# Performance work log

Measured on AMD Instinct MI355X. Metric: run time of the kernel, lower is better.

Reference implementation:

```python
import jax, jax.numpy as jnp
import numpy as np

N_NODES = 100000
N_EDGES = 1600000
N_GRAPHS = 64
IN_DIM, HID, OUT_DIM = 64, 128, 32


def _glorot(key, shape):
    lim = float(np.sqrt(6.0 / (shape[0] + shape[1])))
    return jax.random.uniform(key, shape, jnp.float32, -lim, lim)


def setup_inputs() -> dict:
    key = jax.random.key(0)
    ks = jax.random.split(key, 20)
    x = jax.random.normal(ks[0], (N_NODES, IN_DIM), jnp.float32)
    edge_index = jax.random.randint(ks[1], (2, N_EDGES), 0, N_NODES, jnp.int64)
    batch = jnp.sort(jax.random.randint(ks[2], (N_NODES,), 0, N_GRAPHS, jnp.int64))
    d = {"x": x, "edge_index": edge_index, "batch": batch}
    dims = [(IN_DIM, HID), (HID, HID), (HID, HID), (HID, HID), (HID, OUT_DIM)]
    names = ["W1", "W2", "W3", "W4", "Wo"]
    bnames = ["b1", "b2", "b3", "b4", "bo"]
    for i, ((di, do), wn, bn) in enumerate(zip(dims, names, bnames)):
        d[wn] = _glorot(ks[3 + i], (di, do))
        d[bn] = jnp.zeros((do,), jnp.float32)
    # MLP: 32 -> 64 -> 8 -> 8  (hidden_dim//2, output_dim//2, output_dim//4)
    mdims = [(OUT_DIM, HID // 2), (HID // 2, OUT_DIM // 2), (OUT_DIM // 2, OUT_DIM // 4)]
    for i, (di, do) in enumerate(mdims):
        d[f"M{i+1}w"] = _glorot(ks[10 + i], (di, do))
        d[f"M{i+1}b"] = jnp.zeros((do,), jnp.float32)
    return d


def _gcn(x, src, dst, norm, W, b, n):
    h = x @ W                                    # [N, d_out] dense GEMM
    msg = h[src] * norm[:, None]                 # gather + normalize
    agg = jax.ops.segment_sum(msg, dst, num_segments=n)  # scatter-add
    return agg + b


def reference(x, edge_index, batch, W1, b1, W2, b2, W3, b3, W4, b4, Wo, bo,
              M1w, M1b, M2w, M2b, M3w, M3b):
    n = x.shape[0]
    # add self loops (PyG GCNConv default)
    loops = jnp.arange(n, dtype=edge_index.dtype)
    src = jnp.concatenate([edge_index[0], loops])
    dst = jnp.concatenate([edge_index[1], loops])
    # symmetric degree normalization: D^{-1/2} (A+I) D^{-1/2}
    deg = jax.ops.segment_sum(jnp.ones_like(src, dtype=x.dtype), dst, num_segments=n)
    dinv = jnp.where(deg > 0, jax.lax.rsqrt(deg), 0.0)
    norm = dinv[src] * dinv[dst]                 # [E+N]

    h = jax.nn.relu(_gcn(x, src, dst, norm, W1, b1, n))
    for W, b in ((W2, b2), (W3, b3), (W4, b4)):
        h = jax.nn.relu(_gcn(h, src, dst, norm, W, b, n))
    h = _gcn(h, src, dst, norm, Wo, bo, n)       # [N, 32]

    # global mean pool over graphs
    sums = jax.ops.segment_sum(h, batch, num_segments=N_GRAPHS)
    cnts = jax.ops.segment_sum(jnp.ones((n,), h.dtype), batch, num_segments=N_GRAPHS)
    g = sums / jnp.maximum(cnts, 1.0)[:, None]   # [G, 32]

    g = jax.nn.relu(g @ M1w + M1b)
    g = jax.nn.relu(g @ M2w + M2b)
    return g @ M3w + M3b                          # [G, 8]
```

## Files before the change

kernel.cpp:

```cpp
#include <hip/hip_runtime.h>


static constexpr int TPB = 256;
static constexpr int NBKT = 128;
static constexpr int NCHK = 256;
static constexpr int TILE = 2048;

using f32x4  = __attribute__((ext_vector_type(4))) float;
using bf16x8 = __attribute__((ext_vector_type(8))) short;

__device__ __forceinline__ float u2f(unsigned u) { return __uint_as_float(u); }

__device__ __forceinline__ unsigned short bf1(float a) {
    unsigned u = __float_as_uint(a);
    u += 0x7FFFu + ((u >> 16) & 1u);
    return (unsigned short)(u >> 16);
}

__device__ __forceinline__ unsigned bf2(float a, float b) {
    unsigned ua = __float_as_uint(a);
    unsigned ub = __float_as_uint(b);
    ua += 0x7FFFu + ((ua >> 16) & 1u);
    ub += 0x7FFFu + ((ub >> 16) & 1u);
    return (ua >> 16) | (ub & 0xFFFF0000u);
}

__global__ __launch_bounds__(256) void k_hist(const int* __restrict__ dst,
                                              int* __restrict__ histT, int E, int CS) {
    __shared__ int h[NBKT];
    int c = blockIdx.x, t = threadIdx.x;
    if (t < NBKT) h[t] = 0;
    __syncthreads();
    int e0 = c * CS, e1 = min(e0 + CS, E);
    for (int e = e0 + t; e < e1; e += 256)
        atomicAdd(&h[dst[e] >> 10], 1);
    __syncthreads();
    if (t < NBKT) histT[t * NCHK + c] = h[t];
}

__global__ __launch_bounds__(256) void k_scanS(const int* __restrict__ histT,
                                               int* __restrict__ stg) {
    constexpr int TOT = NBKT * NCHK;
    constexpr int PER = TOT / 256;
    __shared__ int s[256];
    int t = threadIdx.x;
    int base = t * PER;
    int sum = 0;
    for (int i = 0; i < PER; ++i) sum += histT[base + i];
    s[t] = sum;
    __syncthreads();
    for (int off = 1; off < 256; off <<= 1) {
        int add = (t >= off) ? s[t - off] : 0;
        __syncthreads();
        s[t] += add;
        __syncthreads();
    }
    int run = (t > 0) ? s[t - 1] : 0;
    for (int i = 0; i < PER; ++i) {
        stg[base + i] = run;
        run += histT[base + i];
    }
}

__global__ __launch_bounds__(256) void k_bucket(const int* __restrict__ src,
                                                const int* __restrict__ dst,
                                                const int* __restrict__ stg,
                                                unsigned* __restrict__ staging,
                                                int E, int CS) {
    __shared__ int gcur[NBKT];
    __shared__ int cnt_[NBKT];
    __shared__ int base[NBKT];
    __shared__ unsigned sval[TILE];
    __shared__ unsigned char sbkt[TILE];
    int c = blockIdx.x, t = threadIdx.x;
    if (t < NBKT) gcur[t] = stg[t * NCHK + c];
    int e0 = c * CS, e1 = min(e0 + CS, E);

    for (int tb = e0; tb < e1; tb += TILE) {
        int m = min(TILE, e1 - tb);
        __syncthreads();
        if (t < NBKT) cnt_[t] = 0;
        __syncthreads();
        int  b_[8]; unsigned v_[8]; int o_[8]; bool ok_[8];
#pragma unroll
        for (int k = 0; k < 8; ++k) {
            int e = tb + t + k * 256;
            ok_[k] = (e < tb + m);
            b_[k] = 0; v_[k] = 0; o_[k] = 0;
            if (ok_[k]) {
                int d = dst[e];
                b_[k] = d >> 10;
                v_[k] = ((unsigned)src[e] << 10) | (unsigned)(d & 1023);
                o_[k] = atomicAdd(&cnt_[b_[k]], 1);
            }
        }
        __syncthreads();
        if (t < NBKT) base[t] = cnt_[t];
        __syncthreads();
        for (int off = 1; off < NBKT; off <<= 1) {
            int v = (t < NBKT && t >= off) ? base[t - off] : 0;
            __syncthreads();
            if (t < NBKT) base[t] += v;
            __syncthreads();
        }
        if (t < NBKT) base[t] -= cnt_[t];
        __syncthreads();
#pragma unroll
        for (int k = 0; k < 8; ++k) {
            if (ok_[k]) {
                int p = base[b_[k]] + o_[k];
                sval[p] = v_[k];
                sbkt[p] = (unsigned char)b_[k];
            }
        }
        __syncthreads();
        for (int i = t; i < m; i += 256) {
            int b = sbkt[i];
            staging[gcur[b] + (i - base[b])] = sval[i];
        }
        __syncthreads();
        if (t < NBKT) gcur[t] += cnt_[t];
    }
}

__global__ __launch_bounds__(256) void k_deg(const unsigned* __restrict__ staging,
                                             const int* __restrict__ stg,
                                             int* __restrict__ cnt, int E, int n) {
    __shared__ int deg[1024];
    int r = blockIdx.x, t = threadIdx.x;
    for (int i = t; i < 1024; i += 256) deg[i] = 0;
    __syncthreads();
    int s0 = stg[r * NCHK];
    int s1 = (r == NBKT - 1) ? E : stg[(r + 1) * NCHK];
    for (int e = s0 + t; e < s1; e += 256)
        atomicAdd(&deg[staging[e] & 1023u], 1);
    __syncthreads();
    int b = r << 10;
    for (int i = t; i < 1024; i += 256)
        if (b + i < n) cnt[b + i] = deg[i];
}

__global__ void k_scanA(const int* __restrict__ cnt, int* __restrict__ rowptr,
                        int* __restrict__ bsum, int n) {
    __shared__ int s[TPB];
    int t = threadIdx.x;
    int i = blockIdx.x * TPB + t;
    s[t] = (i < n) ? cnt[i] : 0;
    __syncthreads();
    for (int off = 1; off < TPB; off <<= 1) {
        int add = (t >= off) ? s[t - off] : 0;
        __syncthreads();
        s[t] += add;
        __syncthreads();
    }
    if (i < n) rowptr[i + 1] = s[t];
    if (t == TPB - 1) bsum[blockIdx.x] = s[t];
}

__global__ void k_scanB(const int* __restrict__ bsum, int* __restrict__ bscan, int nb) {
    __shared__ int s[512];
    int t = threadIdx.x;
    s[t] = (t < nb) ? bsum[t] : 0;
    __syncthreads();
    for (int off = 1; off < 512; off <<= 1) {
        int add = (t >= off) ? s[t - off] : 0;
        __syncthreads();
        s[t] += add;
        __syncthreads();
    }
    if (t < nb) bscan[t] = (t > 0) ? s[t - 1] : 0;
}

__global__ void k_scanC(int* __restrict__ rowptr, const int* __restrict__ bscan,
                        const int* __restrict__ cnt, float* __restrict__ dinv, int n) {
    int i = blockIdx.x * blockDim.x + threadIdx.x;
    if (i >= n) return;
    rowptr[i + 1] += bscan[i >> 8];
    dinv[i] = rsqrtf((float)cnt[i] + 1.0f);
    if (i == 0) rowptr[0] = 0;
}

__global__ __launch_bounds__(256) void k_fill2(const unsigned* __restrict__ staging,
                                               const int* __restrict__ stg,
                                               const int* __restrict__ rowptr,
                                               int* __restrict__ csr, int E, int n) {
    __shared__ int cur[1024];
    int r = blockIdx.x, t = threadIdx.x;
    int b = r << 10;
    for (int i = t; i < 1024; i += 256)
        cur[i] = (b + i < n) ? rowptr[b + i] : 0;
    __syncthreads();
    int s0 = stg[r * NCHK];
    int s1 = (r == NBKT - 1) ? E : stg[(r + 1) * NCHK];
    for (int e = s0 + t; e < s1; e += 256) {
        unsigned sd = staging[e];
        int p = atomicAdd(&cur[sd & 1023u], 1);
        csr[p] = (int)(sd >> 10);
    }
}

__global__ void k_castx(const float* __restrict__ x, const float* __restrict__ dinv,
                        unsigned short* __restrict__ xs, int n) {
    int gid = blockIdx.x * blockDim.x + threadIdx.x;
    if (gid >= n * 8) return;
    int row = gid >> 3;
    float d = dinv[row];
    const float4* xp = (const float4*)x + (size_t)gid * 2;
    float4 a = xp[0], b = xp[1];
    uint4 o;
    o.x = bf2(a.x * d, a.y * d);
    o.y = bf2(a.z * d, a.w * d);
    o.z = bf2(b.x * d, b.y * d);
    o.w = bf2(b.z * d, b.w * d);
    ((uint4*)xs)[gid] = o;
}

__global__ void k_prepw(const float* __restrict__ W1, const float* __restrict__ W2,
                        const float* __restrict__ W3, const float* __restrict__ W4,
                        const float* __restrict__ Wo,
                        unsigned short* __restrict__ wt1, unsigned short* __restrict__ wt2,
                        unsigned short* __restrict__ wt3, unsigned short* __restrict__ wt4,
                        unsigned short* __restrict__ wto) {
    int b = blockIdx.x, k = threadIdx.x;
    const float* W; unsigned short* wt; int K, OUT, nn;
    if (b < 128)      { W = W1; wt = wt1; K = 64;  OUT = 128; nn = b; }
    else if (b < 256) { W = W2; wt = wt2; K = 128; OUT = 128; nn = b - 128; }
    else if (b < 384) { W = W3; wt = wt3; K = 128; OUT = 128; nn = b - 256; }
    else if (b < 512) { W = W4; wt = wt4; K = 128; OUT = 128; nn = b - 384; }
    else              { W = Wo; wt = wto; K = 128; OUT = 32;  nn = b - 512; }
    if (nn >= OUT || k >= K) return;
    float v = W[(size_t)k * OUT + nn];
    unsigned short hi = bf1(v);
    float fhi = u2f((unsigned)hi << 16);
    unsigned short lo = bf1(v - fhi);
    wt[nn * K + k] = hi;
    wt[OUT * K + nn * K + k] = lo;
}

template <int K, int OUT, int EPI>
__global__ __launch_bounds__(256) void k_gemm_mfma(
    const unsigned short* __restrict__ Ain,
    const unsigned short* __restrict__ WT,
    const float* __restrict__ dinv,
    const float* __restrict__ bias,
    unsigned short* __restrict__ out, int n) {
    constexpr int NT = OUT / 16;
    constexpr int KT = K / 32;
    constexpr int CH = K / 8;
    __shared__ __align__(16) unsigned short Wl[2 * OUT * K];

    int t = threadIdx.x;
    {
        const uint4* wg = (const uint4*)WT;
        uint4* wl = (uint4*)Wl;
        for (int i = t; i < 2 * OUT * CH; i += 256) {
            int m = i / (OUT * CH);
            int r = i - m * (OUT * CH);
            int nn = r / CH, g = r - nn * CH;
            wl[m * OUT * CH + nn * CH + (g ^ (nn & 7))] = wg[i];
        }
    }

    int wid = t >> 6, lane = t & 63;
    int lr = lane & 15, lg = lane >> 4;
    int mbase = blockIdx.x * 128 + wid * 32;

    bf16x8 a[2][KT];
#pragma unroll
    for (int mt = 0; mt < 2; ++mt) {
        int row = mbase + mt * 16 + lr;
        row = row < n ? row : n - 1;
        const bf16x8* ap = (const bf16x8*)(Ain + (size_t)row * K);
#pragma unroll
        for (int kt = 0; kt < KT; ++kt)
            a[mt][kt] = ap[kt * 4 + lg];
    }

    __syncthreads();

    f32x4 acc[2][NT] = {};
#pragma unroll
    for (int nt = 0; nt < NT; ++nt) {
        int nn = nt * 16 + lr;
        int swz = nn & 7;
        int rowoff = nn * K;
#pragma unroll
        for (int kt = 0; kt < KT; ++kt) {
            int g = kt * 4 + lg;
            int off = rowoff + ((g ^ swz) * 8);
            bf16x8 bhi = *(const bf16x8*)&Wl[off];
            bf16x8 blo = *(const bf16x8*)&Wl[OUT * K + off];
#pragma unroll
            for (int mt = 0; mt < 2; ++mt) {
                acc[mt][nt] = __builtin_amdgcn_mfma_f32_16x16x32_bf16(
                    a[mt][kt], bhi, acc[mt][nt], 0, 0, 0);
                acc[mt][nt] = __builtin_amdgcn_mfma_f32_16x16x32_bf16(
                    a[mt][kt], blo, acc[mt][nt], 0, 0, 0);
            }
        }
    }

#pragma unroll
    for (int mt = 0; mt < 2; ++mt) {
        int rbase = mbase + mt * 16 + lg * 4;
        float dv[4];
        if (EPI == 0) {
#pragma unroll
            for (int r = 0; r < 4; ++r)
                dv[r] = (rbase + r < n) ? dinv[rbase + r] : 0.f;
        }
#pragma unroll
        for (int nt = 0; nt < NT; ++nt) {
            int col = nt * 16 + lr;
            float bb = (EPI == 1) ? bias[col] : 0.f;
#pragma unroll
            for (int r = 0; r < 4; ++r) {
                int row = rbase + r;
                if (row < n) {
                    float v = acc[mt][nt][r];
                    if (EPI == 0) v *= dv[r];
                    else v = fmaxf(v + bb, 0.f);
                    out[(size_t)row * OUT + col] = bf1(v);
                }
            }
        }
    }
}

__device__ __forceinline__ void addbf(float* acc, uint4 w) {
    acc[0] += u2f(w.x << 16); acc[1] += u2f(w.x & 0xFFFF0000u);
    acc[2] += u2f(w.y << 16); acc[3] += u2f(w.y & 0xFFFF0000u);
    acc[4] += u2f(w.z << 16); acc[5] += u2f(w.z & 0xFFFF0000u);
    acc[6] += u2f(w.w << 16); acc[7] += u2f(w.w & 0xFFFF0000u);
}

template <int D, bool RELU, bool HASBIAS, bool OUTBF>
__global__ __launch_bounds__(256) void k_gather_bf(const unsigned short* __restrict__ hsb,
                                                   const int* __restrict__ rowptr,
                                                   const int* __restrict__ csr,
                                                   const float* __restrict__ dinv,
                                                   const float* __restrict__ bias,
                                                   void* __restrict__ outp, int n) {
    constexpr int TPN = D / 8;
    int gid = blockIdx.x * blockDim.x + threadIdx.x;
    int node = gid / TPN;
    if (node >= n) return;
    int c = gid % TPN;
    const uint4* hb = (const uint4*)hsb;

    float acc[8];
    {
        uint4 v = hb[(size_t)node * TPN + c];
        acc[0] = u2f(v.x << 16); acc[1] = u2f(v.x & 0xFFFF0000u);
        acc[2] = u2f(v.y << 16); acc[3] = u2f(v.y & 0xFFFF0000u);
        acc[4] = u2f(v.z << 16); acc[5] = u2f(v.z & 0xFFFF0000u);
        acc[6] = u2f(v.w << 16); acc[7] = u2f(v.w & 0xFFFF0000u);
    }
    int j0 = rowptr[node], j1 = rowptr[node + 1];
    int j = j0;
    for (; j + 3 < j1; j += 4) {
        int s0 = csr[j], s1 = csr[j + 1], s2 = csr[j + 2], s3 = csr[j + 3];
        uint4 w0 = hb[(size_t)s0 * TPN + c];
        uint4 w1 = hb[(size_t)s1 * TPN + c];
        uint4 w2 = hb[(size_t)s2 * TPN + c];
        uint4 w3 = hb[(size_t)s3 * TPN + c];
        addbf(acc, w0); addbf(acc, w1); addbf(acc, w2); addbf(acc, w3);
    }
    for (; j < j1; ++j) {
        uint4 w0 = hb[(size_t)csr[j] * TPN + c];
        addbf(acc, w0);
    }

    float di = dinv[node];
    float r[8];
    if (HASBIAS) {
        float4 b0 = *(const float4*)&bias[c * 8];
        float4 b1 = *(const float4*)&bias[c * 8 + 4];
        r[0] = di * acc[0] + b0.x; r[1] = di * acc[1] + b0.y;
        r[2] = di * acc[2] + b0.z; r[3] = di * acc[3] + b0.w;
        r[4] = di * acc[4] + b1.x; r[5] = di * acc[5] + b1.y;
        r[6] = di * acc[6] + b1.z; r[7] = di * acc[7] + b1.w;
    } else {
#pragma unroll
        for (int i = 0; i < 8; ++i) r[i] = di * acc[i];
    }
    if (RELU) {
#pragma unroll
        for (int i = 0; i < 8; ++i) r[i] = fmaxf(r[i], 0.f);
    }
    if (OUTBF) {
        uint4 o;
        o.x = bf2(r[0], r[1]); o.y = bf2(r[2], r[3]);
        o.z = bf2(r[4], r[5]); o.w = bf2(r[6], r[7]);
        ((uint4*)outp)[(size_t)node * TPN + c] = o;
    } else {
        float4 o0 = {r[0], r[1], r[2], r[3]};
        float4 o1 = {r[4], r[5], r[6], r[7]};
        float4* op = (float4*)outp + (size_t)node * TPN * 2 + c * 2;
        op[0] = o0;
        op[1] = o1;
    }
}

__global__ __launch_bounds__(256) void k_pool(const float* __restrict__ h,
                                              const int* __restrict__ batch,
                                              float* __restrict__ g, int n) {
    __shared__ int se[2];
    __shared__ float red[8][32];
    int gi = blockIdx.x;
    int t = threadIdx.x;
    if (t == 0) {
        int lo = 0, hi = n;
        while (lo < hi) { int m = (lo + hi) >> 1; if (batch[m] < gi) lo = m + 1; else hi = m; }
        se[0] = lo;
        lo = 0; hi = n;
        while (lo < hi) { int m = (lo + hi) >> 1; if (batch[m] < gi + 1) lo = m + 1; else hi = m; }
        se[1] = lo;
    }
    __syncthreads();
    int start = se[0], end = se[1];
    int col = t & 31, sub = t >> 5;
    float acc = 0.f;
    for (int i = start + sub; i < end; i += 8)
        acc += h[(size_t)i * 32 + col];
    red[sub][col] = acc;
    __syncthreads();
    if (t < 32) {
        float s = 0.f;
#pragma unroll
        for (int q = 0; q < 8; ++q) s += red[q][t];
        float c = (float)(end - start);
        g[gi * 32 + t] = s / fmaxf(c, 1.0f);
    }
}

template <int K, int O, bool RELU>
__global__ void k_mlp(const float* __restrict__ in, const float* __restrict__ W,
                      const float* __restrict__ b, float* __restrict__ out, int G) {
    int gid = blockIdx.x * blockDim.x + threadIdx.x;
    if (gid >= G * O) return;
    int g = gid / O, j = gid % O;
    float s = b[j];
    for (int k = 0; k < K; ++k) s += in[g * K + k] * W[k * O + j];
    if (RELU) s = fmaxf(s, 0.f);
    out[gid] = s;
}

extern "C" void kernel_launch(void* const* d_in, const int* in_sizes, int n_in,
                              void* d_out, int out_size, void* d_ws, size_t ws_size,
                              hipStream_t stream) {
    const float* x    = (const float*)d_in[0];
    const int*   ei   = (const int*)d_in[1];
    const int*   batch= (const int*)d_in[2];
    const float* W1 = (const float*)d_in[3];  const float* b1 = (const float*)d_in[4];
    const float* W2 = (const float*)d_in[5];  const float* b2 = (const float*)d_in[6];
    const float* W3 = (const float*)d_in[7];  const float* b3 = (const float*)d_in[8];
    const float* W4 = (const float*)d_in[9];  const float* b4 = (const float*)d_in[10];
    const float* Wo = (const float*)d_in[11]; const float* bo = (const float*)d_in[12];
    const float* M1w = (const float*)d_in[13]; const float* M1b = (const float*)d_in[14];
    const float* M2w = (const float*)d_in[15]; const float* M2b = (const float*)d_in[16];
    const float* M3w = (const float*)d_in[17]; const float* M3b = (const float*)d_in[18];

    const int N = in_sizes[0] / 64;
    const int E = in_sizes[1] / 2;
    const int G = out_size / 8;
    const int* src  = ei;
    const int* dstp = ei + E;

    char* w = (char*)d_ws;
    unsigned short* buf1 = (unsigned short*)w; w += (size_t)N * 128 * 2;
    unsigned short* buf2 = (unsigned short*)w; w += (size_t)N * 128 * 4;
    unsigned short* hsb  = (unsigned short*)w; w += (size_t)N * 128 * 2;
    int*      csr     = (int*)w;      w += (size_t)E * 4;
    unsigned* staging = (unsigned*)w; w += (size_t)E * 4;
    int*      histT   = (int*)w;      w += NBKT * NCHK * 4;
    int*      stg     = (int*)w;      w += NBKT * NCHK * 4;
    int*      cnt     = (int*)w;      w += (size_t)N * 4;
    int*      rowptr  = (int*)w;      w += (size_t)(N + 4) * 4;
    int*      bsum    = (int*)w;      w += 4096;
    int*      bscan   = (int*)w;      w += 4096;
    float*    dinv    = (float*)w;    w += (size_t)N * 4;
    unsigned short* wt1 = (unsigned short*)w; w += 2 * 128 * 64 * 2;
    unsigned short* wt2 = (unsigned short*)w; w += 2 * 128 * 128 * 2;
    unsigned short* wt3 = (unsigned short*)w; w += 2 * 128 * 128 * 2;
    unsigned short* wt4 = (unsigned short*)w; w += 2 * 128 * 128 * 2;
    unsigned short* wto = (unsigned short*)w; w += 2 * 32 * 128 * 2;
    float*    gp      = (float*)w;    w += 64 * 32 * 4;
    float*    m1      = (float*)w;    w += 64 * 64 * 4;
    float*    m2      = (float*)w;    w += 64 * 16 * 4;

    const int NB = (N + TPB - 1) / TPB;
    const int CS = (E + NCHK - 1) / NCHK;
    const int GB = (N + 127) / 128;

    k_hist<<<NCHK, 256, 0, stream>>>(dstp, histT, E, CS);
    k_prepw<<<544, 128, 0, stream>>>(W1, W2, W3, W4, Wo, wt1, wt2, wt3, wt4, wto);
    k_scanS<<<1, 256, 0, stream>>>(histT, stg);
    k_bucket<<<NCHK, 256, 0, stream>>>(src, dstp, stg, staging, E, CS);
    k_deg<<<NBKT, 256, 0, stream>>>(staging, stg, cnt, E, N);
    k_scanA<<<NB, TPB, 0, stream>>>(cnt, rowptr, bsum, N);
    k_scanB<<<1, 512, 0, stream>>>(bsum, bscan, NB);
    k_scanC<<<NB, TPB, 0, stream>>>(rowptr, bscan, cnt, dinv, N);
    k_fill2<<<NBKT, 256, 0, stream>>>(staging, stg, rowptr, csr, E, N);

    unsigned short* agg = buf1;
    unsigned short* xs  = buf2;

    k_castx<<<(N * 8 + 255) / 256, 256, 0, stream>>>(x, dinv, xs, N);
    k_gather_bf<64, false, false, true><<<(N * 8 + 255) / 256, 256, 0, stream>>>(
        xs, rowptr, csr, dinv, nullptr, agg, N);
    k_gemm_mfma<64, 128, 1><<<GB, 256, 0, stream>>>(agg, wt1, nullptr, b1, buf2, N);

    k_gemm_mfma<128, 128, 0><<<GB, 256, 0, stream>>>(buf2, wt2, dinv, nullptr, hsb, N);
    k_gather_bf<128, true, true, true><<<(N * 16 + 255) / 256, 256, 0, stream>>>(
        hsb, rowptr, csr, dinv, b2, buf1, N);
    k_gemm_mfma<128, 128, 0><<<GB, 256, 0, stream>>>(buf1, wt3, dinv, nullptr, hsb, N);
    k_gather_bf<128, true, true, true><<<(N * 16 + 255) / 256, 256, 0, stream>>>(
        hsb, rowptr, csr, dinv, b3, buf2, N);
    k_gemm_mfma<128, 128, 0><<<GB, 256, 0, stream>>>(buf2, wt4, dinv, nullptr, hsb, N);
    k_gather_bf<128, true, true, true><<<(N * 16 + 255) / 256, 256, 0, stream>>>(
        hsb, rowptr, csr, dinv, b4, buf1, N);

    k_gemm_mfma<128, 32, 0><<<GB, 256, 0, stream>>>(buf1, wto, dinv, nullptr, hsb, N);
    float* hout = (float*)buf2;
    k_gather_bf<32, false, true, false><<<(N * 4 + 255) / 256, 256, 0, stream>>>(
        hsb, rowptr, csr, dinv, bo, hout, N);

    k_pool<<<G, 256, 0, stream>>>(hout, batch, gp, N);
    k_mlp<32, 64, true><<<(G * 64 + 255) / 256, 256, 0, stream>>>(gp, M1w, M1b, m1, G);
    k_mlp<64, 16, true><<<(G * 16 + 255) / 256, 256, 0, stream>>>(m1, M2w, M2b, m2, G);
    k_mlp<16, 8, false><<<(G * 8 + 255) / 256, 256, 0, stream>>>(m2, M3w, M3b, (float*)d_out, G);
}
```

Measured before the change: 628.8 us.

## Fuse CSR build into one kernel and use XCD-restricted persistent gather queue

Merges degree counting, the three-pass prefix scan and CSR fill into a single k_build kernel. This works because each bucket's node range is contiguous and its edge offset is already known from stg, so the scan can be done locally per block. It also replaces the one-thread-per-feature-chunk gather kernels with a persistent atomic work-queue kernel. Most blocks running on XCDs with ID 4 or higher exit immediately, so the gathers are intended to run on half the XCDs, which should improve L2 locality of the gathered feature rows. The risks are fewer compute units doing gather work, contention on the queue atomic, and reliance on the XCC_ID hardware register.

```diff
diff --git a/kernel.cpp b/kernel.cpp
--- a/kernel.cpp
+++ b/kernel.cpp
@@ -5,6 +5,8 @@
 static constexpr int NBKT = 128;
 static constexpr int NCHK = 256;
 static constexpr int TILE = 2048;
+static constexpr int GQ_GRID = 2048;
+static constexpr int GQ_FS   = GQ_GRID - 256;
 
 using f32x4  = __attribute__((ext_vector_type(4))) float;
 using bf16x8 = __attribute__((ext_vector_type(8))) short;
@@ -123,10 +125,13 @@
     }
 }
 
-__global__ __launch_bounds__(256) void k_deg(const unsigned* __restrict__ staging,
-                                             const int* __restrict__ stg,
-                                             int* __restrict__ cnt, int E, int n) {
+__global__ __launch_bounds__(256) void k_build(const unsigned* __restrict__ staging,
+                                               const int* __restrict__ stg,
+                                               int* __restrict__ rowptr,
+                                               float* __restrict__ dinv,
+                                               int* __restrict__ csr, int E, int n) {
     __shared__ int deg[1024];
+    __shared__ int tsum[256];
     int r = blockIdx.x, t = threadIdx.x;
     for (int i = t; i < 1024; i += 256) deg[i] = 0;
     __syncthreads();
@@ -135,66 +140,30 @@
     for (int e = s0 + t; e < s1; e += 256)
         atomicAdd(&deg[staging[e] & 1023u], 1);
     __syncthreads();
+    int d0 = deg[t * 4], d1 = deg[t * 4 + 1], d2 = deg[t * 4 + 2], d3 = deg[t * 4 + 3];
+    tsum[t] = d0 + d1 + d2 + d3;
+    __syncthreads();
+    for (int off = 1; off < 256; off <<= 1) {
+        int v = (t >= off) ? tsum[t - off] : 0;
+        __syncthreads();
+        tsum[t] += v;
+        __syncthreads();
+    }
+    int o0 = s0 + ((t > 0) ? tsum[t - 1] : 0);
+    int o1 = o0 + d0, o2 = o1 + d1, o3 = o2 + d2;
     int b = r << 10;
-    for (int i = t; i < 1024; i += 256)
-        if (b + i < n) cnt[b + i] = deg[i];
-}
-
-__global__ void k_scanA(const int* __restrict__ cnt, int* __restrict__ rowptr,
-                        int* __restrict__ bsum, int n) {
-    __shared__ int s[TPB];
-    int t = threadIdx.x;
-    int i = blockIdx.x * TPB + t;
-    s[t] = (i < n) ? cnt[i] : 0;
-    __syncthreads();
-    for (int off = 1; off < TPB; off <<= 1) {
-        int add = (t >= off) ? s[t - off] : 0;
-        __syncthreads();
-        s[t] += add;
-        __syncthreads();
-    }
-    if (i < n) rowptr[i + 1] = s[t];
-    if (t == TPB - 1) bsum[blockIdx.x] = s[t];
-}
-
-__global__ void k_scanB(const int* __restrict__ bsum, int* __restrict__ bscan, int nb) {
-    __shared__ int s[512];
-    int t = threadIdx.x;
-    s[t] = (t < nb) ? bsum[t] : 0;
-    __syncthreads();
-    for (int off = 1; off < 512; off <<= 1) {
-        int add = (t >= off) ? s[t - off] : 0;
-        __syncthreads();
-        s[t] += add;
-        __syncthreads();
-    }
-    if (t < nb) bscan[t] = (t > 0) ? s[t - 1] : 0;
-}
-
-__global__ void k_scanC(int* __restrict__ rowptr, const int* __restrict__ bscan,
-                        const int* __restrict__ cnt, float* __restrict__ dinv, int n) {
-    int i = blockIdx.x * blockDim.x + threadIdx.x;
-    if (i >= n) return;
-    rowptr[i + 1] += bscan[i >> 8];
-    dinv[i] = rsqrtf((float)cnt[i] + 1.0f);
-    if (i == 0) rowptr[0] = 0;
-}
-
-__global__ __launch_bounds__(256) void k_fill2(const unsigned* __restrict__ staging,
-                                               const int* __restrict__ stg,
-                                               const int* __restrict__ rowptr,
-                                               int* __restrict__ csr, int E, int n) {
-    __shared__ int cur[1024];
-    int r = blockIdx.x, t = threadIdx.x;
-    int b = r << 10;
-    for (int i = t; i < 1024; i += 256)
-        cur[i] = (b + i < n) ? rowptr[b + i] : 0;
-    __syncthreads();
-    int s0 = stg[r * NCHK];
-    int s1 = (r == NBKT - 1) ? E : stg[(r + 1) * NCHK];
+    int nd = b + t * 4;
+    if (nd + 0 < n) { rowptr[nd + 0] = o0; dinv[nd + 0] = rsqrtf((float)d0 + 1.f); }
+    if (nd + 1 < n) { rowptr[nd + 1] = o1; dinv[nd + 1] = rsqrtf((float)d1 + 1.f); }
+    if (nd + 2 < n) { rowptr[nd + 2] = o2; dinv[nd + 2] = rsqrtf((float)d2 + 1.f); }
+    if (nd + 3 < n) { rowptr[nd + 3] = o3; dinv[nd + 3] = rsqrtf((float)d3 + 1.f); }
+    if (r == 0 && t == 0) rowptr[n] = E;
+    __syncthreads();
+    deg[t * 4] = o0; deg[t * 4 + 1] = o1; deg[t * 4 + 2] = o2; deg[t * 4 + 3] = o3;
+    __syncthreads();
     for (int e = s0 + t; e < s1; e += 256) {
         unsigned sd = staging[e];
-        int p = atomicAdd(&cur[sd & 1023u], 1);
+        int p = atomicAdd(&deg[sd & 1023u], 1);
         csr[p] = (int)(sd >> 10);
     }
 }
@@ -334,71 +303,88 @@
     acc[6] += u2f(w.w << 16); acc[7] += u2f(w.w & 0xFFFF0000u);
 }
 
-template <int D, bool RELU, bool HASBIAS, bool OUTBF>
-__global__ __launch_bounds__(256) void k_gather_bf(const unsigned short* __restrict__ hsb,
-                                                   const int* __restrict__ rowptr,
-                                                   const int* __restrict__ csr,
-                                                   const float* __restrict__ dinv,
-                                                   const float* __restrict__ bias,
-                                                   void* __restrict__ outp, int n) {
+template <int D, bool RELU, bool HASBIAS, bool OUTBF, int NXCD>
+__global__ __launch_bounds__(256) void k_gather_q(
+    const unsigned short* __restrict__ hsb,
+    const int* __restrict__ rowptr, const int* __restrict__ csr,
+    const float* __restrict__ dinv, const float* __restrict__ bias,
+    void* __restrict__ outp, int* __restrict__ qctr, int n, int nitems) {
     constexpr int TPN = D / 8;
-    int gid = blockIdx.x * blockDim.x + threadIdx.x;
-    int node = gid / TPN;
-    if (node >= n) return;
-    int c = gid % TPN;
+    constexpr int NPB = 256 / TPN;
+    constexpr int NSTR = 2;
+    constexpr int ITEM = NPB * NSTR;
+    __shared__ int sitem;
+    unsigned xcc;
+    asm volatile("s_getreg_b32 %0, hwreg(HW_REG_XCC_ID)" : "=s"(xcc));
+    if ((int)(xcc & 7) >= NXCD && blockIdx.x < GQ_FS) return;
+    int t = threadIdx.x;
+    int c = t % TPN;
+    int nl = t / TPN;
     const uint4* hb = (const uint4*)hsb;
 
-    float acc[8];
-    {
-        uint4 v = hb[(size_t)node * TPN + c];
-        acc[0] = u2f(v.x << 16); acc[1] = u2f(v.x & 0xFFFF0000u);
-        acc[2] = u2f(v.y << 16); acc[3] = u2f(v.y & 0xFFFF0000u);
-        acc[4] = u2f(v.z << 16); acc[5] = u2f(v.z & 0xFFFF0000u);
-        acc[6] = u2f(v.w << 16); acc[7] = u2f(v.w & 0xFFFF0000u);
-    }
-    int j0 = rowptr[node], j1 = rowptr[node + 1];
-    int j = j0;
-    for (; j + 3 < j1; j += 4) {
-        int s0 = csr[j], s1 = csr[j + 1], s2 = csr[j + 2], s3 = csr[j + 3];
-        uint4 w0 = hb[(size_t)s0 * TPN + c];
-        uint4 w1 = hb[(size_t)s1 * TPN + c];
-        uint4 w2 = hb[(size_t)s2 * TPN + c];
-        uint4 w3 = hb[(size_t)s3 * TPN + c];
-        addbf(acc, w0); addbf(acc, w1); addbf(acc, w2); addbf(acc, w3);
-    }
-    for (; j < j1; ++j) {
-        uint4 w0 = hb[(size_t)csr[j] * TPN + c];
-        addbf(acc, w0);
-    }
-
-    float di = dinv[node];
-    float r[8];
-    if (HASBIAS) {
-        float4 b0 = *(const float4*)&bias[c * 8];
-        float4 b1 = *(const float4*)&bias[c * 8 + 4];
-        r[0] = di * acc[0] + b0.x; r[1] = di * acc[1] + b0.y;
-        r[2] = di * acc[2] + b0.z; r[3] = di * acc[3] + b0.w;
-        r[4] = di * acc[4] + b1.x; r[5] = di * acc[5] + b1.y;
-        r[6] = di * acc[6] + b1.z; r[7] = di * acc[7] + b1.w;
-    } else {
-#pragma unroll
-        for (int i = 0; i < 8; ++i) r[i] = di * acc[i];
-    }
-    if (RELU) {
-#pragma unroll
-        for (int i = 0; i < 8; ++i) r[i] = fmaxf(r[i], 0.f);
-    }
-    if (OUTBF) {
-        uint4 o;
-        o.x = bf2(r[0], r[1]); o.y = bf2(r[2], r[3]);
-        o.z = bf2(r[4], r[5]); o.w = bf2(r[6], r[7]);
-        ((uint4*)outp)[(size_t)node * TPN + c] = o;
-    } else {
-        float4 o0 = {r[0], r[1], r[2], r[3]};
-        float4 o1 = {r[4], r[5], r[6], r[7]};
-        float4* op = (float4*)outp + (size_t)node * TPN * 2 + c * 2;
-        op[0] = o0;
-        op[1] = o1;
+    for (;;) {
+        if (t == 0) sitem = atomicAdd(qctr, 1);
+        __syncthreads();
+        int item = sitem;
+        __syncthreads();
+        if (item >= nitems) return;
+#pragma unroll
+        for (int s = 0; s < NSTR; ++s) {
+            int node = item * ITEM + s * NPB + nl;
+            if (node >= n) continue;
+            float acc[8];
+            {
+                uint4 v = hb[(size_t)node * TPN + c];
+                acc[0] = u2f(v.x << 16); acc[1] = u2f(v.x & 0xFFFF0000u);
+                acc[2] = u2f(v.y << 16); acc[3] = u2f(v.y & 0xFFFF0000u);
+                acc[4] = u2f(v.z << 16); acc[5] = u2f(v.z & 0xFFFF0000u);
+                acc[6] = u2f(v.w << 16); acc[7] = u2f(v.w & 0xFFFF0000u);
+            }
+            int j0 = rowptr[node], j1 = rowptr[node + 1];
+            int j = j0;
+            for (; j + 3 < j1; j += 4) {
+                int s0 = csr[j], s1 = csr[j + 1], s2 = csr[j + 2], s3 = csr[j + 3];
+                uint4 w0 = hb[(size_t)s0 * TPN + c];
+                uint4 w1 = hb[(size_t)s1 * TPN + c];
+                uint4 w2 = hb[(size_t)s2 * TPN + c];
+                uint4 w3 = hb[(size_t)s3 * TPN + c];
+                addbf(acc, w0); addbf(acc, w1); addbf(acc, w2); addbf(acc, w3);
+            }
+            for (; j < j1; ++j) {
+                uint4 w0 = hb[(size_t)csr[j] * TPN + c];
+                addbf(acc, w0);
+            }
+
+            float di = dinv[node];
+            float r[8];
+            if (HASBIAS) {
+                float4 b0 = *(const float4*)&bias[c * 8];
+                float4 b1 = *(const float4*)&bias[c * 8 + 4];
+                r[0] = di * acc[0] + b0.x; r[1] = di * acc[1] + b0.y;
+                r[2] = di * acc[2] + b0.z; r[3] = di * acc[3] + b0.w;
+                r[4] = di * acc[4] + b1.x; r[5] = di * acc[5] + b1.y;
+                r[6] = di * acc[6] + b1.z; r[7] = di * acc[7] + b1.w;
+            } else {
+#pragma unroll
+                for (int i = 0; i < 8; ++i) r[i] = di * acc[i];
+            }
+            if (RELU) {
+#pragma unroll
+                for (int i = 0; i < 8; ++i) r[i] = fmaxf(r[i], 0.f);
+            }
+            if (OUTBF) {
+                uint4 o;
+                o.x = bf2(r[0], r[1]); o.y = bf2(r[2], r[3]);
+                o.z = bf2(r[4], r[5]); o.w = bf2(r[6], r[7]);
+                ((uint4*)outp)[(size_t)node * TPN + c] = o;
+            } else {
+                float4 o0 = {r[0], r[1], r[2], r[3]};
+                float4 o1 = {r[4], r[5], r[6], r[7]};
+                float4* op = (float4*)outp + (size_t)node * TPN * 2 + c * 2;
+                op[0] = o0;
+                op[1] = o1;
+            }
+        }
     }
 }
 
@@ -475,11 +461,9 @@
     unsigned* staging = (unsigned*)w; w += (size_t)E * 4;
     int*      histT   = (int*)w;      w += NBKT * NCHK * 4;
     int*      stg     = (int*)w;      w += NBKT * NCHK * 4;
-    int*      cnt     = (int*)w;      w += (size_t)N * 4;
     int*      rowptr  = (int*)w;      w += (size_t)(N + 4) * 4;
-    int*      bsum    = (int*)w;      w += 4096;
-    int*      bscan   = (int*)w;      w += 4096;
     float*    dinv    = (float*)w;    w += (size_t)N * 4;
+    int*      qctr    = (int*)w;      w += 64;
     unsigned short* wt1 = (unsigned short*)w; w += 2 * 128 * 64 * 2;
     unsigned short* wt2 = (unsigned short*)w; w += 2 * 128 * 128 * 2;
     unsigned short* wt3 = (unsigned short*)w; w += 2 * 128 * 128 * 2;
@@ -489,42 +473,41 @@
     float*    m1      = (float*)w;    w += 64 * 64 * 4;
     float*    m2      = (float*)w;    w += 64 * 16 * 4;
 
-    const int NB = (N + TPB - 1) / TPB;
     const int CS = (E + NCHK - 1) / NCHK;
     const int GB = (N + 127) / 128;
-
+    const int NI128 = (N + 31) / 32;
+    const int NI64  = (N + 63) / 64;
+    const int NI32  = (N + 127) / 128;
+
+    hipMemsetAsync(qctr, 0, 64, stream);
     k_hist<<<NCHK, 256, 0, stream>>>(dstp, histT, E, CS);
     k_prepw<<<544, 128, 0, stream>>>(W1, W2, W3, W4, Wo, wt1, wt2, wt3, wt4, wto);
     k_scanS<<<1, 256, 0, stream>>>(histT, stg);
     k_bucket<<<NCHK, 256, 0, stream>>>(src, dstp, stg, staging, E, CS);
-    k_deg<<<NBKT, 256, 0, stream>>>(staging, stg, cnt, E, N);
-    k_scanA<<<NB, TPB, 0, stream>>>(cnt, rowptr, bsum, N);
-    k_scanB<<<1, 512, 0, stream>>>(bsum, bscan, NB);
-    k_scanC<<<NB, TPB, 0, stream>>>(rowptr, bscan, cnt, dinv, N);
-    k_fill2<<<NBKT, 256, 0, stream>>>(staging, stg, rowptr, csr, E, N);
+    k_build<<<NBKT, 256, 0, stream>>>(staging, stg, rowptr, dinv, csr, E, N);
 
     unsigned short* agg = buf1;
     unsigned short* xs  = buf2;
 
     k_castx<<<(N * 8 + 255) / 256, 256, 0, stream>>>(x, dinv, xs, N);
-    k_gather_bf<64, false, false, true><<<(N * 8 + 255) / 256, 256, 0, stream>>>(
-        xs, rowptr, csr, dinv, nullptr, agg, N);
+    k_gather_q<64, false, false, true, 4><<<GQ_GRID, 256, 0, stream>>>(
+        xs, rowptr, csr, dinv, nullptr, agg, qctr + 0, N, NI64);
     k_gemm_mfma<64, 128, 1><<<GB, 256, 0, stream>>>(agg, wt1, nullptr, b1, buf2, N);
 
     k_gemm_mfma<128, 128, 0><<<GB, 256, 0, stream>>>(buf2, wt2, dinv, nullptr, hsb, N);
-    k_gather_bf<128, true, true, true><<<(N * 16 + 255) / 256, 256, 0, stream>>>(
-        hsb, rowptr, csr, dinv, b2, buf1, N);
+    k_gather_q<128, true, true, true, 4><<<GQ_GRID, 256, 0, stream>>>(
+        hsb, rowptr, csr, dinv, b2, buf1, qctr + 1, N, NI128);
     k_gemm_mfma<128, 128, 0><<<GB, 256, 0, stream>>>(buf1, wt3, dinv, nullptr, hsb, N);
-    k_gather_bf<128, true, true, true><<<(N * 16 + 255) / 256, 256, 0, stream>>>(
-        hsb, rowptr, csr, dinv, b3, buf2, N);
+    k_gather_q<128, true, true, true, 4><<<GQ_GRID, 256, 0, stream>>>(
+        hsb, rowptr, csr, dinv, b3, buf2, qctr + 2, N, NI128);
     k_gemm_mfma<128, 128, 0><<<GB, 256, 0, stream>>>(buf2, wt4, dinv, nullptr, hsb, N);
-    k_gather_bf<128, true, true, true><<<(N * 16 + 255) / 256, 256, 0, stream>>>(
-        hsb, rowptr, csr, dinv, b4, buf1, N);
+    k_gather_q<128, true, true, true, 4><<<GQ_GRID, 256, 0, stream>>>(
+        hsb, rowptr, csr, dinv, b4, buf1, qctr + 3, N, NI128);
 
     k_gemm_mfma<128, 32, 0><<<GB, 256, 0, stream>>>(buf1, wto, dinv, nullptr, hsb, N);
     float* hout = (float*)buf2;
-    k_gather_bf<32, false, true, false><<<(N * 4 + 255) / 256, 256, 0, stream>>>(
-        hsb, rowptr, csr, dinv, bo, hout, N);
+    k_gather_q<32, false, true, false, 4><<<GQ_GRID, 256, 0, stream>>>(
+        hsb, rowptr, csr, dinv, bo, hout, qctr + 4, N, NI32);
 
     k_pool<<<G, 256, 0, stream>>>(hout, batch, gp, N);
     k_mlp<32, 64, true><<<(G * 64 + 255) / 256, 256, 0, stream>>>(gp, M1w, M1b, m1, G);
```

New measurement: 813.3 us. 29.3% more time.
